# Optimization experiments

Hardware: AMD Instinct MI355X
Metric: run time of the kernel (lower is better)

Reference implementation:

```python
import jax, jax.numpy as jnp
import numpy as np

N_Q = 6        # qubits per circuit
N_CL = 32      # entangler layers per circuit
N_MOD = 32     # number of qlayer modules (feature parts)
PART = 64      # 2048 // 32

# Pauli-Z sign table: state flattened as (B, 2**N_Q) with wire 0 the most
# significant axis; signs[k, i] = (-1)**bit_i(k).
_bits = (np.arange(2 ** N_Q)[:, None] >> np.arange(N_Q - 1, -1, -1)[None, :]) & 1
SIGNS = jnp.asarray(1.0 - 2.0 * _bits, dtype=jnp.float32)  # [64, 6]


def _apply_1q(state, gate, wire):
    # state: [B, 2, 2, 2, 2, 2, 2] complex64; gate: [2, 2]
    axis = 1 + wire
    state = jnp.tensordot(gate, state, axes=((1,), (axis,)))
    return jnp.moveaxis(state, 0, axis)


def _apply_cnot(state, ctrl, tgt):
    ci, ti = 1 + ctrl, 1 + tgt
    s0 = jax.lax.index_in_dim(state, 0, ci, keepdims=True)
    s1 = jax.lax.index_in_dim(state, 1, ci, keepdims=True)
    return jnp.concatenate([s0, jnp.flip(s1, axis=ti)], axis=ci)


def _rx(theta):
    c = jnp.cos(theta * 0.5).astype(jnp.complex64)
    s = jnp.sin(theta * 0.5).astype(jnp.complex64)
    return jnp.stack([jnp.stack([c, -1j * s]), jnp.stack([-1j * s, c])])


def _circuit(angles, weights):
    # angles: [B, 6] (AngleEmbedding RY params); weights: [N_CL, 6] (RX params)
    B = angles.shape[0]
    half = angles * 0.5
    # RY(a)|0> = cos(a/2)|0> + sin(a/2)|1>  -> product state
    amps = jnp.stack([jnp.cos(half), jnp.sin(half)], axis=-1).astype(jnp.complex64)  # [B,6,2]
    state = amps[:, 0]
    for q in range(1, N_Q):
        state = state[..., None] * amps[:, q].reshape((B,) + (1,) * q + (2,))
    # state: [B,2,2,2,2,2,2]

    def layer(st, w):
        # BasicEntanglerLayers: RX on every wire, then ring of CNOTs
        for q in range(N_Q):
            st = _apply_1q(st, _rx(w[q]), q)
        for q in range(N_Q):
            st = _apply_cnot(st, q, (q + 1) % N_Q)
        return st, None

    state, _ = jax.lax.scan(jax.checkpoint(layer), state, weights)
    probs = (state.real ** 2 + state.imag ** 2).reshape(B, 2 ** N_Q)
    return probs @ SIGNS  # [B, 6] expvals of PauliZ on each wire


def _forward(features, Wp, bp, qw, Wf, bf):
    B = features.shape[0]
    parts = features.reshape(B, N_MOD, PART)                 # 32 chunks of 64
    angles = jnp.einsum('bpd,qd->bpq', parts, Wp) + bp       # shared projector -> [B,32,6]
    outs = jax.vmap(_circuit, in_axes=(1, 0), out_axes=1)(angles, qw)  # [B,32,6]
    return outs.reshape(B, N_MOD * N_Q) @ Wf.T + bf          # [B, num_classes]


def setup_inputs() -> dict:
    key = jax.random.key(0)
    k1, k2, k3, k4 = jax.random.split(key, 4)
    B, num_classes = 2048, 150
    features = jax.random.normal(k1, (B, 2048), dtype=jnp.float32)
    Wp = jax.random.normal(k2, (N_Q, PART), dtype=jnp.float32) * (1.0 / np.sqrt(PART))
    bp = jnp.zeros((N_Q,), dtype=jnp.float32)
    qw = jax.random.uniform(k3, (N_MOD, N_CL, N_Q), dtype=jnp.float32) * (2.0 * np.pi)
    Wf = jax.random.normal(k4, (num_classes, N_MOD * N_Q), dtype=jnp.float32) * (1.0 / np.sqrt(N_MOD * N_Q))
    bf = jnp.zeros((num_classes,), dtype=jnp.float32)
    return {'features': features, 'Wp': Wp, 'bp': bp, 'qw': qw, 'Wf': Wf, 'bf': bf}


def reference(features, Wp, bp, qw, Wf, bf):
    return _forward(features, Wp, bp, qw, Wf, bf)
```

## Files before the change

### kernel.cpp

```cpp
#include <hip/hip_runtime.h>

#define NQ   6
#define DIM  64
#define NMOD 32
#define NCL  32
#define BATCH 2048
#define NCLS 150
#define KF   192
#define NROWS (BATCH*NMOD)

#define OFF_CSTAB 0
#define OFF_U2    12288
#define OFF_CAMPS 274432
#define OFF_OUTS  1060864

__global__ __launch_bounds__(256) void k_cstab(const float* __restrict__ qw,
                                               float* __restrict__ cstab) {
    int i = blockIdx.x * 256 + threadIdx.x;
    if (i < NMOD * NCL * NQ) {
        float s, c;
        sincosf(0.5f * qw[i], &s, &c);
        cstab[2 * i + 0] = c;
        cstab[2 * i + 1] = s;
    }
}

__global__ __launch_bounds__(192) void k_angles(const float* __restrict__ features,
                                                const float* __restrict__ Wp,
                                                const float* __restrict__ bp,
                                                float* __restrict__ camps) {
    __shared__ float ldsA[64 * 33];
    __shared__ float ldsW[NQ * 64];
    int tid = threadIdx.x;
    int rowbase = blockIdx.x * 32;
    const float* src = features + (size_t)rowbase * 64;
    for (int idx = tid; idx < 32 * 64; idx += 192) {
        int r = idx >> 6, d = idx & 63;
        ldsA[d * 33 + r] = src[idx];
    }
    for (int idx = tid; idx < NQ * 64; idx += 192) ldsW[idx] = Wp[idx];
    __syncthreads();

    int q = tid >> 5;
    int r = tid & 31;
    float acc = 0.f;
#pragma unroll
    for (int d = 0; d < 64; ++d) acc += ldsA[d * 33 + r] * ldsW[q * 64 + d];
    float half = 0.5f * (acc + bp[q]);
    float s, c;
    sincosf(half, &s, &c);
    int row = rowbase + r;
    camps[(row * NQ + q) * 2 + 0] = c;
    camps[(row * NQ + q) * 2 + 1] = s;
}

__global__ __launch_bounds__(256) void k_unitary(const float* __restrict__ cstab,
                                                 float* __restrict__ U2f) {
    int tid = threadIdx.x;
    int lane = tid & 63;
    int w = tid >> 6;
    int p = blockIdx.x >> 4;
    int col = ((blockIdx.x & 15) << 2) + w;

    float re = (lane == col) ? 1.f : 0.f;
    float im = 0.f;
    const float* cs = cstab + p * NCL * NQ * 2;

    for (int layer = 0; layer < NCL; ++layer) {
        const float* lw = cs + layer * NQ * 2;
#pragma unroll
        for (int q = 0; q < NQ; ++q) {
            float c = lw[2 * q], s = lw[2 * q + 1];
            int mask = 1 << (5 - q);
            float pre = __shfl_xor(re, mask, 64);
            float pim = __shfl_xor(im, mask, 64);
            float nre = fmaf(c, re, s * pim);
            float nim = fmaf(c, im, -s * pre);
            re = nre;
            im = nim;
        }
#pragma unroll
        for (int q = 0; q < NQ; ++q) {
            int cmask = 1 << (5 - q);
            int tmask = 1 << (5 - ((q + 1) % 6));
            float pre = __shfl_xor(re, tmask, 64);
            float pim = __shfl_xor(im, tmask, 64);
            bool ctrl = (lane & cmask) != 0;
            re = ctrl ? pre : re;
            im = ctrl ? pim : im;
        }
    }
    float2* dst = (float2*)U2f;
    dst[p * (DIM * DIM) + col * DIM + lane] = make_float2(re, im);
}

__global__ __launch_bounds__(256) void k_circuit(const float* __restrict__ camps,
                                                 const float* __restrict__ U2f,
                                                 float* __restrict__ outs) {
    __shared__ float psi[4][64][8];
    int tid = threadIdx.x;
    int lane = tid & 63;
    int w = tid >> 6;
    int p = blockIdx.x & 31;
    int btile = blockIdx.x >> 5;
    int b0 = btile * 32 + w * 8;

    float pv[8];
#pragma unroll
    for (int bi = 0; bi < 8; ++bi) {
        int row = (b0 + bi) * NMOD + p;
        const float* ca = camps + row * NQ * 2;
        float v = 1.f;
#pragma unroll
        for (int q = 0; q < NQ; ++q) {
            float c = ca[2 * q], s = ca[2 * q + 1];
            v *= ((lane >> (5 - q)) & 1) ? s : c;
        }
        pv[bi] = v;
    }
    *(float4*)&psi[w][lane][0] = make_float4(pv[0], pv[1], pv[2], pv[3]);
    *(float4*)&psi[w][lane][4] = make_float4(pv[4], pv[5], pv[6], pv[7]);
    __syncthreads();

    const float2* U = (const float2*)U2f + p * (DIM * DIM);
    float yre[8], yim[8];
#pragma unroll
    for (int bi = 0; bi < 8; ++bi) { yre[bi] = 0.f; yim[bi] = 0.f; }

#pragma unroll 8
    for (int col = 0; col < 64; ++col) {
        float2 u = U[col * 64 + lane];
        float pc[8];
        *(float4*)&pc[0] = *(const float4*)&psi[w][col][0];
        *(float4*)&pc[4] = *(const float4*)&psi[w][col][4];
#pragma unroll
        for (int bi = 0; bi < 8; ++bi) {
            yre[bi] = fmaf(u.x, pc[bi], yre[bi]);
            yim[bi] = fmaf(u.y, pc[bi], yim[bi]);
        }
    }

    float sgn[6];
#pragma unroll
    for (int k = 0; k < 6; ++k) sgn[k] = ((lane >> k) & 1) ? -1.f : 1.f;

#pragma unroll
    for (int bi = 0; bi < 8; ++bi) {
        float v = yre[bi] * yre[bi] + yim[bi] * yim[bi];
#pragma unroll
        for (int k = 0; k < 6; ++k) {
            float t = __shfl_xor(v, 1 << k, 64);
            v = fmaf(sgn[k], v, t);
        }
        if (lane != 0 && (lane & (lane - 1)) == 0) {
            int bpos = __ffs(lane) - 1;
            int q = 5 - bpos;
            outs[(b0 + bi) * KF + p * NQ + q] = v;
        }
    }
}

__global__ __launch_bounds__(256) void k_final(const float* __restrict__ outs,
                                               const float* __restrict__ Wf,
                                               const float* __restrict__ bf,
                                               float* __restrict__ out) {
    int tid = threadIdx.x;
    int b = blockIdx.x * 64 + (tid & 63);
    int c = blockIdx.y * 4 + (tid >> 6);
    if (c >= NCLS) return;
    float acc = bf[c];
    const float* orow = outs + b * KF;
    const float* wrow = Wf + c * KF;
#pragma unroll
    for (int k = 0; k < KF; k += 4) {
        float4 o = *(const float4*)&orow[k];
        float4 wv = *(const float4*)&wrow[k];
        acc = fmaf(o.x, wv.x, acc);
        acc = fmaf(o.y, wv.y, acc);
        acc = fmaf(o.z, wv.z, acc);
        acc = fmaf(o.w, wv.w, acc);
    }
    out[b * NCLS + c] = acc;
}

extern "C" void kernel_launch(void* const* d_in, const int* in_sizes, int n_in,
                              void* d_out, int out_size, void* d_ws, size_t ws_size,
                              hipStream_t stream) {
    const float* features = (const float*)d_in[0];
    const float* Wp       = (const float*)d_in[1];
    const float* bp       = (const float*)d_in[2];
    const float* qw       = (const float*)d_in[3];
    const float* Wf       = (const float*)d_in[4];
    const float* bf       = (const float*)d_in[5];
    float* out = (float*)d_out;
    float* ws  = (float*)d_ws;

    float* cstab = ws + OFF_CSTAB;
    float* U2    = ws + OFF_U2;
    float* camps = ws + OFF_CAMPS;
    float* outsb = ws + OFF_OUTS;

    k_cstab<<<(NMOD * NCL * NQ + 255) / 256, 256, 0, stream>>>(qw, cstab);
    k_angles<<<NROWS / 32, 192, 0, stream>>>(features, Wp, bp, camps);
    k_unitary<<<NMOD * 16, 256, 0, stream>>>(cstab, U2);
    k_circuit<<<NMOD * (BATCH / 32), 256, 0, stream>>>(camps, U2, outsb);
    k_final<<<dim3(BATCH / 64, (NCLS + 3) / 4), 256, 0, stream>>>(outsb, Wf, bf, out);
}
```

Before: 161.3 us.

## Fuse RX table into unitary build, permute-CNOTs, restructure circuit matvec per batch lane

```diff
diff --git a/kernel.cpp b/kernel.cpp
--- a/kernel.cpp
+++ b/kernel.cpp
@@ -9,21 +9,9 @@
 #define KF   192
 #define NROWS (BATCH*NMOD)
 
-#define OFF_CSTAB 0
-#define OFF_U2    12288
-#define OFF_CAMPS 274432
-#define OFF_OUTS  1060864
-
-__global__ __launch_bounds__(256) void k_cstab(const float* __restrict__ qw,
-                                               float* __restrict__ cstab) {
-    int i = blockIdx.x * 256 + threadIdx.x;
-    if (i < NMOD * NCL * NQ) {
-        float s, c;
-        sincosf(0.5f * qw[i], &s, &c);
-        cstab[2 * i + 0] = c;
-        cstab[2 * i + 1] = s;
-    }
-}
+#define OFF_UT    0
+#define OFF_CAMPS 262144
+#define OFF_OUTS  1048576
 
 __global__ __launch_bounds__(192) void k_angles(const float* __restrict__ features,
                                                 const float* __restrict__ Wp,
@@ -54,109 +42,130 @@
     camps[(row * NQ + q) * 2 + 1] = s;
 }
 
-__global__ __launch_bounds__(256) void k_unitary(const float* __restrict__ cstab,
-                                                 float* __restrict__ U2f) {
+__global__ __launch_bounds__(256) void k_prep(const float* __restrict__ qw,
+                                              float* __restrict__ UTf) {
+    __shared__ float2 csl[NCL * NQ];
     int tid = threadIdx.x;
     int lane = tid & 63;
     int w = tid >> 6;
     int p = blockIdx.x >> 4;
     int col = ((blockIdx.x & 15) << 2) + w;
 
+    if (tid < NCL * NQ) {
+        float s, c;
+        sincosf(0.5f * qw[p * NCL * NQ + tid], &s, &c);
+        csl[tid] = make_float2(c, s);
+    }
+    __syncthreads();
+
+    int dst = lane;
+#pragma unroll
+    for (int q = 0; q < NQ; ++q) {
+        int cm = 1 << (5 - q), tm = 1 << (5 - ((q + 1) % 6));
+        dst ^= (dst & cm) ? tm : 0;
+    }
+    int dst_b = dst << 2;
+
     float re = (lane == col) ? 1.f : 0.f;
     float im = 0.f;
-    const float* cs = cstab + p * NCL * NQ * 2;
 
     for (int layer = 0; layer < NCL; ++layer) {
-        const float* lw = cs + layer * NQ * 2;
 #pragma unroll
         for (int q = 0; q < NQ; ++q) {
-            float c = lw[2 * q], s = lw[2 * q + 1];
+            float2 cs = csl[layer * NQ + q];
             int mask = 1 << (5 - q);
             float pre = __shfl_xor(re, mask, 64);
             float pim = __shfl_xor(im, mask, 64);
-            float nre = fmaf(c, re, s * pim);
-            float nim = fmaf(c, im, -s * pre);
+            float nre = fmaf(cs.x, re, cs.y * pim);
+            float nim = fmaf(cs.x, im, -cs.y * pre);
             re = nre;
             im = nim;
         }
-#pragma unroll
-        for (int q = 0; q < NQ; ++q) {
-            int cmask = 1 << (5 - q);
-            int tmask = 1 << (5 - ((q + 1) % 6));
-            float pre = __shfl_xor(re, tmask, 64);
-            float pim = __shfl_xor(im, tmask, 64);
-            bool ctrl = (lane & cmask) != 0;
-            re = ctrl ? pre : re;
-            im = ctrl ? pim : im;
-        }
-    }
-    float2* dst = (float2*)U2f;
-    dst[p * (DIM * DIM) + col * DIM + lane] = make_float2(re, im);
-}
-
-__global__ __launch_bounds__(256) void k_circuit(const float* __restrict__ camps,
-                                                 const float* __restrict__ U2f,
-                                                 float* __restrict__ outs) {
-    __shared__ float psi[4][64][8];
+        re = __int_as_float(__builtin_amdgcn_ds_permute(dst_b, __float_as_int(re)));
+        im = __int_as_float(__builtin_amdgcn_ds_permute(dst_b, __float_as_int(im)));
+    }
+    float2* UT2 = (float2*)UTf;
+    UT2[p * (DIM * DIM) + lane * DIM + col] = make_float2(re, im);
+}
+
+__global__ __launch_bounds__(256, 4) void k_circuit(const float* __restrict__ camps,
+                                                    const float* __restrict__ UTf,
+                                                    float* __restrict__ outs) {
+    __shared__ float zl[4][5][64];
     int tid = threadIdx.x;
     int lane = tid & 63;
     int w = tid >> 6;
+    int wq = __builtin_amdgcn_readfirstlane(w);
     int p = blockIdx.x & 31;
     int btile = blockIdx.x >> 5;
-    int b0 = btile * 32 + w * 8;
-
-    float pv[8];
-#pragma unroll
-    for (int bi = 0; bi < 8; ++bi) {
-        int row = (b0 + bi) * NMOD + p;
-        const float* ca = camps + row * NQ * 2;
-        float v = 1.f;
-#pragma unroll
-        for (int q = 0; q < NQ; ++q) {
-            float c = ca[2 * q], s = ca[2 * q + 1];
-            v *= ((lane >> (5 - q)) & 1) ? s : c;
+    int b = btile * 64 + lane;
+
+    float ca[12];
+    {
+        const float4* cp = (const float4*)(camps + (size_t)(b * NMOD + p) * NQ * 2);
+        float4 c0 = cp[0], c1 = cp[1], c2 = cp[2];
+        ca[0] = c0.x; ca[1] = c0.y; ca[2] = c0.z; ca[3] = c0.w;
+        ca[4] = c1.x; ca[5] = c1.y; ca[6] = c1.z; ca[7] = c1.w;
+        ca[8] = c2.x; ca[9] = c2.y; ca[10] = c2.z; ca[11] = c2.w;
+    }
+
+    float psi[DIM];
+    psi[0] = 1.f;
+#pragma unroll
+    for (int q = 5; q >= 0; --q) {
+        int sz = 1 << (5 - q);
+        float c = ca[2 * q], s = ca[2 * q + 1];
+#pragma unroll
+        for (int k = 0; k < 64; ++k) {
+            if (k < sz) {
+                psi[k + sz] = psi[k] * s;
+                psi[k] = psi[k] * c;
+            }
         }
-        pv[bi] = v;
-    }
-    *(float4*)&psi[w][lane][0] = make_float4(pv[0], pv[1], pv[2], pv[3]);
-    *(float4*)&psi[w][lane][4] = make_float4(pv[4], pv[5], pv[6], pv[7]);
+    }
+
+    float ps = 0.f, z2 = 0.f, z3 = 0.f, z4 = 0.f, z5 = 0.f;
+    const float4* Ubase = (const float4*)(UTf + (size_t)p * DIM * DIM * 2);
+
+#pragma unroll
+    for (int ii = 0; ii < 16; ++ii) {
+        int i = wq * 16 + ii;
+        const float4* Ur = Ubase + i * 32;
+        float yre = 0.f, yim = 0.f;
+#pragma unroll
+        for (int j4 = 0; j4 < 32; ++j4) {
+            float4 u = Ur[j4];
+            yre = fmaf(u.x, psi[2 * j4], yre);
+            yim = fmaf(u.y, psi[2 * j4], yim);
+            yre = fmaf(u.z, psi[2 * j4 + 1], yre);
+            yim = fmaf(u.w, psi[2 * j4 + 1], yim);
+        }
+        float prob = fmaf(yre, yre, yim * yim);
+        ps += prob;
+        z2 += (ii & 8) ? -prob : prob;
+        z3 += (ii & 4) ? -prob : prob;
+        z4 += (ii & 2) ? -prob : prob;
+        z5 += (ii & 1) ? -prob : prob;
+    }
+
+    zl[w][0][lane] = ps;
+    zl[w][1][lane] = z2;
+    zl[w][2][lane] = z3;
+    zl[w][3][lane] = z4;
+    zl[w][4][lane] = z5;
     __syncthreads();
 
-    const float2* U = (const float2*)U2f + p * (DIM * DIM);
-    float yre[8], yim[8];
-#pragma unroll
-    for (int bi = 0; bi < 8; ++bi) { yre[bi] = 0.f; yim[bi] = 0.f; }
-
-#pragma unroll 8
-    for (int col = 0; col < 64; ++col) {
-        float2 u = U[col * 64 + lane];
-        float pc[8];
-        *(float4*)&pc[0] = *(const float4*)&psi[w][col][0];
-        *(float4*)&pc[4] = *(const float4*)&psi[w][col][4];
-#pragma unroll
-        for (int bi = 0; bi < 8; ++bi) {
-            yre[bi] = fmaf(u.x, pc[bi], yre[bi]);
-            yim[bi] = fmaf(u.y, pc[bi], yim[bi]);
-        }
-    }
-
-    float sgn[6];
-#pragma unroll
-    for (int k = 0; k < 6; ++k) sgn[k] = ((lane >> k) & 1) ? -1.f : 1.f;
-
-#pragma unroll
-    for (int bi = 0; bi < 8; ++bi) {
-        float v = yre[bi] * yre[bi] + yim[bi] * yim[bi];
-#pragma unroll
-        for (int k = 0; k < 6; ++k) {
-            float t = __shfl_xor(v, 1 << k, 64);
-            v = fmaf(sgn[k], v, t);
-        }
-        if (lane != 0 && (lane & (lane - 1)) == 0) {
-            int bpos = __ffs(lane) - 1;
-            int q = 5 - bpos;
-            outs[(b0 + bi) * KF + p * NQ + q] = v;
-        }
+    if (tid < 64) {
+        float p0 = zl[0][0][tid], p1 = zl[1][0][tid], p2 = zl[2][0][tid], p3 = zl[3][0][tid];
+        float z0 = (p0 + p1) - (p2 + p3);
+        float z1 = (p0 - p1) + (p2 - p3);
+        float o2 = zl[0][1][tid] + zl[1][1][tid] + zl[2][1][tid] + zl[3][1][tid];
+        float o3 = zl[0][2][tid] + zl[1][2][tid] + zl[2][2][tid] + zl[3][2][tid];
+        float o4 = zl[0][3][tid] + zl[1][3][tid] + zl[2][3][tid] + zl[3][3][tid];
+        float o5 = zl[0][4][tid] + zl[1][4][tid] + zl[2][4][tid] + zl[3][4][tid];
+        int bb = btile * 64 + tid;
+        float* o = outs + (size_t)bb * KF + p * NQ;
+        o[0] = z0; o[1] = z1; o[2] = o2; o[3] = o3; o[4] = o4; o[5] = o5;
     }
 }
 
@@ -169,8 +178,8 @@
     int c = blockIdx.y * 4 + (tid >> 6);
     if (c >= NCLS) return;
     float acc = bf[c];
-    const float* orow = outs + b * KF;
-    const float* wrow = Wf + c * KF;
+    const float* orow = outs + (size_t)b * KF;
+    const float* wrow = Wf + (size_t)c * KF;
 #pragma unroll
     for (int k = 0; k < KF; k += 4) {
         float4 o = *(const float4*)&orow[k];
@@ -195,14 +204,12 @@
     float* out = (float*)d_out;
     float* ws  = (float*)d_ws;
 
-    float* cstab = ws + OFF_CSTAB;
-    float* U2    = ws + OFF_U2;
+    float* UT    = ws + OFF_UT;
     float* camps = ws + OFF_CAMPS;
     float* outsb = ws + OFF_OUTS;
 
-    k_cstab<<<(NMOD * NCL * NQ + 255) / 256, 256, 0, stream>>>(qw, cstab);
     k_angles<<<NROWS / 32, 192, 0, stream>>>(features, Wp, bp, camps);
-    k_unitary<<<NMOD * 16, 256, 0, stream>>>(cstab, U2);
-    k_circuit<<<NMOD * (BATCH / 32), 256, 0, stream>>>(camps, U2, outsb);
+    k_prep<<<NMOD * 16, 256, 0, stream>>>(qw, UT);
+    k_circuit<<<NMOD * (BATCH / 64), 256, 0, stream>>>(camps, UT, outsb);
     k_final<<<dim3(BATCH / 64, (NCLS + 3) / 4), 256, 0, stream>>>(outsb, Wf, bf, out);
 }
```

Result: no change. 164.2 us (+1.8%).
